# Kernel tuning notes

Measured on AMD Instinct MI355X. Metric: run time of the kernel, lower is better.

The kernel has to match this reference:

```python
import jax, jax.numpy as jnp
import numpy as np


def setup_inputs() -> dict:
    key = jax.random.key(0)
    kx, kq, kk, kv = jax.random.split(key, 4)
    B, S, F, D = 4, 4096, 512, 64
    x = jax.random.normal(kx, (B, S, F), dtype=jnp.float32)
    Wq = jax.random.normal(kq, (F, D), dtype=jnp.float32) * 0.05
    Wk = jax.random.normal(kk, (F, D), dtype=jnp.float32) * 0.05
    Wv = jax.random.normal(kv, (F, D), dtype=jnp.float32) * 0.05
    return {"x": x, "Wq": Wq, "Wk": Wk, "Wv": Wv}


def reference(x, Wq, Wk, Wv):
    # x: [B,S,F]; Wq/Wk/Wv: [F,D]
    q = jnp.einsum('bsf,fd->bsd', x, Wq)
    k = jnp.einsum('bsf,fd->bsd', x, Wk)
    v = jnp.einsum('bsf,fd->bsd', x, Wv)
    scale = 1.0 / jnp.sqrt(jnp.asarray(Wq.shape[-1], dtype=x.dtype))
    scores = jnp.einsum('bqd,bkd->bqk', q, k) * scale  # [B,S,S]
    weights = jax.nn.softmax(scores, axis=-1)
    return jnp.einsum('bqk,bkd->bqd', weights, v)
```

## Files before the change

### kernel.cpp

```cpp
#include <hip/hip_runtime.h>

constexpr int Bc = 4, Sc = 4096, Fc = 512, Dc = 64;
constexpr int SPLIT = 8;
constexpr int KT = 64;
constexpr int TILES = (Sc / SPLIT) / KT;

typedef __attribute__((ext_vector_type(8)))  short  short8;
typedef __attribute__((ext_vector_type(4)))  float  float4v;
typedef __attribute__((ext_vector_type(16))) float  float16v;
typedef __attribute__((ext_vector_type(2)))  unsigned int uint2v;

__device__ inline unsigned short f2bf(float f) {
    union { float f; unsigned u; } v; v.f = f;
    unsigned r = v.u + 0x7FFF + ((v.u >> 16) & 1);
    return (unsigned short)(r >> 16);
}
__device__ inline unsigned pk2(float a, float b) {
    union { float f; unsigned u; } x, y; x.f = a; y.f = b;
    unsigned ra = x.u + 0x7FFF + ((x.u >> 16) & 1);
    unsigned rb = y.u + 0x7FFF + ((y.u >> 16) & 1);
    return (ra >> 16) | (rb & 0xFFFF0000u);
}
__device__ inline unsigned cvtpk2(float lo, float hi) {
    unsigned r;
    asm("v_cvt_pk_bf16_f32 %0, %1, %2" : "=v"(r) : "v"(lo), "v"(hi));
    return r;
}
__device__ inline float exp2fast(float x) {
#if defined(__has_builtin) && __has_builtin(__builtin_amdgcn_exp2f)
    return __builtin_amdgcn_exp2f(x);
#else
    return __expf(x * 0.69314718055994531f);
#endif
}

__device__ inline void swap32(unsigned& a, unsigned& b) {
#if defined(__has_builtin) && __has_builtin(__builtin_amdgcn_permlane32_swap)
    uint2v r = __builtin_amdgcn_permlane32_swap(a, b, false, false);
    a = r[0]; b = r[1];
#else
    unsigned ax = (unsigned)__shfl_xor((int)a, 32);
    unsigned bx = (unsigned)__shfl_xor((int)b, 32);
    int upper = (threadIdx.x & 32) != 0;
    unsigned na = upper ? bx : a;
    unsigned nb = upper ? b  : ax;
    a = na; b = nb;
#endif
}

__global__ __launch_bounds__(256) void prep_kernel(
    const float* __restrict__ Wq, const float* __restrict__ Wk,
    const float* __restrict__ Wv, unsigned short* __restrict__ Wf)
{
    int wi = blockIdx.x * 256 + threadIdx.x;
    int lane = wi & 63;
    int kc = (wi >> 6) & 15;
    int nt = wi >> 10;
    int lm = lane & 15, quad = lane >> 4;
    int n = nt * 16 + lm;
    const float* W = (n < 64) ? Wq : (n < 128) ? Wk : Wv;
    int nc = n & 63;
    float scale = (n < 64) ? 0.18033688011112042f : 1.0f;
    int kbase = kc * 32 + quad * 8;
    union { uint4 v; unsigned short s[8]; } tmp;
    #pragma unroll
    for (int j = 0; j < 8; ++j)
        tmp.s[j] = f2bf(W[(size_t)(kbase + j) * Dc + nc] * scale);
    *(uint4*)&Wf[(size_t)wi * 8] = tmp.v;
}

__global__ __launch_bounds__(256) void qkv_kernel(
    const float* __restrict__ x, const unsigned short* __restrict__ Wf,
    unsigned short* __restrict__ Qb, unsigned short* __restrict__ Kb,
    unsigned short* __restrict__ Vtb)
{
    __shared__ __align__(16) unsigned short Xs[2][16][72];
    __shared__ __align__(16) unsigned short Ot[16][200];
    const int t = threadIdx.x;
    const int lane = t & 63, w = t >> 6;
    const int lm = lane & 15, quad = lane >> 4;
    const int row0 = blockIdx.x * 16;
    const int sr = t >> 4, sc4 = (t & 15) * 4;

    float4 xv;
    auto load_x = [&](int k0) {
        xv = *(const float4*)&x[(size_t)(row0 + sr) * Fc + k0 + sc4];
    };
    load_x(0);

    float4v acc[3];
    #pragma unroll
    for (int n = 0; n < 3; ++n) acc[n] = float4v{0.f, 0.f, 0.f, 0.f};

    int buf = 0;
    #pragma unroll
    for (int k0 = 0; k0 < Fc; k0 += 64, buf ^= 1) {
        uint2 pk;
        pk.x = pk2(xv.x, xv.y); pk.y = pk2(xv.z, xv.w);
        *(uint2*)&Xs[buf][sr][sc4] = pk;
        __syncthreads();
        if (k0 + 64 < Fc) load_x(k0 + 64);

        short8 af[2];
        #pragma unroll
        for (int h = 0; h < 2; ++h)
            af[h] = *(const short8*)&Xs[buf][lm][h * 32 + quad * 8];

        #pragma unroll
        for (int n = 0; n < 3; ++n) {
            const int nt = 3 * w + n;
            #pragma unroll
            for (int h = 0; h < 2; ++h) {
                const int kchunk = (k0 >> 5) + h;
                short8 bf_ = *(const short8*)&Wf[(size_t)((nt * 16 + kchunk) * 64 + lane) * 8];
                acc[n] = __builtin_amdgcn_mfma_f32_16x16x32_bf16(af[h], bf_, acc[n], 0, 0, 0);
            }
        }
    }

    __syncthreads();
    #pragma unroll
    for (int n = 0; n < 3; ++n)
        #pragma unroll
        for (int r = 0; r < 4; ++r)
            Ot[quad * 4 + r][(3 * w + n) * 16 + lm] = f2bf(acc[n][r]);
    __syncthreads();

    {
        const int r2 = t >> 4, c2 = (t & 15) * 4;
        *(uint2*)&Qb[(size_t)(row0 + r2) * Dc + c2] = *(const uint2*)&Ot[r2][c2];
        *(uint2*)&Kb[(size_t)(row0 + r2) * Dc + c2] = *(const uint2*)&Ot[r2][64 + c2];
    }
    {
        const int d = t >> 2, s4 = (t & 3) * 4;
        union { uint2 v; unsigned short s[4]; } tmp;
        #pragma unroll
        for (int j = 0; j < 4; ++j) tmp.s[j] = Ot[s4 + j][128 + d];
        const int bb = row0 >> 12, s0r = row0 & (Sc - 1);
        *(uint2*)&Vtb[((size_t)bb * Dc + d) * Sc + s0r + s4] = tmp.v;
    }
}

__global__ __launch_bounds__(256) void attn_kernel(
    const unsigned short* __restrict__ Qb, const unsigned short* __restrict__ Kb,
    const unsigned short* __restrict__ Vtb,
    float* __restrict__ Op, float* __restrict__ lp)
{
    __shared__ __align__(16) char smem[34816];

    const int t = threadIdx.x;
    const int lane = t & 63, w = t >> 6;
    const int l31 = lane & 31, lh = lane >> 5;
    const int b = blockIdx.y, z = blockIdx.z;
    const int q0 = blockIdx.x * 128 + w * 32;
    const size_t qkbase = (size_t)b * Sc * Dc;
    const size_t vbase  = (size_t)b * Dc * Sc;
    const int k0base = z * (Sc / SPLIT);

    short8 qf[4];
    #pragma unroll
    for (int c = 0; c < 4; ++c)
        qf[c] = *(const short8*)&Qb[qkbase + (size_t)(q0 + l31) * Dc + c * 16 + lh * 8];

    float16v O0, O1;
    #pragma unroll
    for (int r = 0; r < 16; ++r) { O0[r] = 0.f; O1[r] = 0.f; }
    float lA = 0.f, lB = 0.f;

    const int rowInW = lane >> 3;
    const int srcChunk = (lane & 7) ^ rowInW;
    auto stage = [&](int p, int k0) {
        char* base = smem + p * 16384;
        #pragma unroll
        for (int j = 0; j < 2; ++j) {
            const int row = w * 16 + j * 8 + rowInW;
            const unsigned short* gk = Kb + qkbase + (size_t)(k0 + row) * Dc + srcChunk * 8;
            const unsigned short* gv = Vtb + vbase + (size_t)row * Sc + k0 + srcChunk * 8;
            __builtin_amdgcn_global_load_lds(
                (const __attribute__((address_space(1))) void*)gk,
                (__attribute__((address_space(3))) void*)(base + (w * 16 + j * 8) * 128),
                16, 0, 0);
            __builtin_amdgcn_global_load_lds(
                (const __attribute__((address_space(1))) void*)gv,
                (__attribute__((address_space(3))) void*)(base + 8192 + (w * 16 + j * 8) * 128),
                16, 0, 0);
        }
    };

    const int rx = l31 & 7;
    auto rd = [&](const char* buf, int row, int cc) -> short8 {
        return *(const short8*)(buf + row * 128 + (cc ^ rx) * 16);
    };

    auto mk_pb = [&](const float16v& s, int g) -> short8 {
        unsigned X0 = cvtpk2(s[8 * g + 0], s[8 * g + 1]);
        unsigned X1 = cvtpk2(s[8 * g + 2], s[8 * g + 3]);
        unsigned Y0 = cvtpk2(s[8 * g + 4], s[8 * g + 5]);
        unsigned Y1 = cvtpk2(s[8 * g + 6], s[8 * g + 7]);
        swap32(X0, Y0);
        swap32(X1, Y1);
        union { unsigned u[4]; short8 s8; } r;
        r.u[0] = X0; r.u[1] = X1; r.u[2] = Y0; r.u[3] = Y1;
        return r.s8;
    };

    stage(0, k0base);
    __syncthreads();

    int p = 0;
    for (int kt = 0; kt < TILES; ++kt, p ^= 1) {
        if (kt + 1 < TILES) stage(p ^ 1, k0base + (kt + 1) * KT);
        const char* kb = smem + p * 16384;
        const char* vb = kb + 8192;

        float16v s0, s1;
        #pragma unroll
        for (int r = 0; r < 16; ++r) { s0[r] = 0.f; s1[r] = 0.f; }
        __builtin_amdgcn_s_setprio(1);
        #pragma unroll
        for (int c = 0; c < 4; ++c) {
            short8 a0 = rd(kb, l31,      2 * c + lh);
            short8 a1 = rd(kb, 32 + l31, 2 * c + lh);
            s0 = __builtin_amdgcn_mfma_f32_32x32x16_bf16(a0, qf[c], s0, 0, 0, 0);
            s1 = __builtin_amdgcn_mfma_f32_32x32x16_bf16(a1, qf[c], s1, 0, 0, 0);
        }
        __builtin_amdgcn_s_setprio(0);

        #pragma unroll
        for (int r = 0; r < 16; ++r) {
            float p0 = exp2fast(s0[r]); s0[r] = p0; lA += p0;
            float p1 = exp2fast(s1[r]); s1[r] = p1; lB += p1;
        }

        short8 pb0 = mk_pb(s0, 0);
        short8 pb1 = mk_pb(s0, 1);
        short8 pb2 = mk_pb(s1, 0);
        short8 pb3 = mk_pb(s1, 1);

        __builtin_amdgcn_s_setprio(1);
        #pragma unroll
        for (int c = 0; c < 4; ++c) {
            short8 pb  = (c == 0) ? pb0 : (c == 1) ? pb1 : (c == 2) ? pb2 : pb3;
            short8 va0 = rd(vb, l31,      2 * c + lh);
            short8 va1 = rd(vb, 32 + l31, 2 * c + lh);
            O0 = __builtin_amdgcn_mfma_f32_32x32x16_bf16(va0, pb, O0, 0, 0, 0);
            O1 = __builtin_amdgcn_mfma_f32_32x32x16_bf16(va1, pb, O1, 0, 0, 0);
        }
        __builtin_amdgcn_s_setprio(0);

        __syncthreads();
    }

    float l_i = lA + lB;
    l_i += __shfl_xor(l_i, 32);

    float* Of = (float*)(smem + w * 8704);
    #pragma unroll
    for (int r = 0; r < 16; ++r) {
        int d0 = (r & 3) + 8 * (r >> 2) + 4 * lh;
        Of[l31 * 68 + d0]      = O0[r];
        Of[l31 * 68 + 32 + d0] = O1[r];
    }
    const size_t obase = ((size_t)(z * Bc + b) * Sc + q0) * Dc;
    const int qr = lane >> 4, c4 = (lane & 15) * 4;
    #pragma unroll
    for (int i = 0; i < 8; ++i) {
        int q = i * 4 + qr;
        *(float4*)&Op[obase + (size_t)q * Dc + c4] = *(const float4*)&Of[q * 68 + c4];
    }
    if (lane < 32)
        lp[(z * Bc + b) * Sc + q0 + l31] = l_i;
}

__global__ __launch_bounds__(256) void combine_kernel(
    const float* __restrict__ Op, const float* __restrict__ lp,
    float* __restrict__ out)
{
    const int BS = Bc * Sc;
    int tid = blockIdx.x * 256 + threadIdx.x;
    int bq = tid >> 4, dc = (tid & 15) * 4;
    float L = 0.f;
    #pragma unroll
    for (int zz = 0; zz < SPLIT; ++zz) L += lp[zz * BS + bq];
    float inv = 1.f / L;
    size_t o = (size_t)bq * Dc + dc;
    size_t stride = (size_t)BS * Dc;
    float4 r = {0.f, 0.f, 0.f, 0.f};
    #pragma unroll
    for (int zz = 0; zz < SPLIT; ++zz) {
        float4 pz = *(const float4*)&Op[o + zz * stride];
        r.x += pz.x; r.y += pz.y; r.z += pz.z; r.w += pz.w;
    }
    r.x *= inv; r.y *= inv; r.z *= inv; r.w *= inv;
    *(float4*)&out[o] = r;
}

extern "C" void kernel_launch(void* const* d_in, const int* in_sizes, int n_in,
                              void* d_out, int out_size, void* d_ws, size_t ws_size,
                              hipStream_t stream) {
    const float* x  = (const float*)d_in[0];
    const float* Wq = (const float*)d_in[1];
    const float* Wk = (const float*)d_in[2];
    const float* Wv = (const float*)d_in[3];
    float* out = (float*)d_out;

    char* p = (char*)d_ws;
    unsigned short* Wf  = (unsigned short*)p;  p += (size_t)192 * Fc * 2;
    unsigned short* Qb  = (unsigned short*)p;  p += (size_t)Bc * Sc * Dc * 2;
    unsigned short* Kb  = (unsigned short*)p;  p += (size_t)Bc * Sc * Dc * 2;
    unsigned short* Vtb = (unsigned short*)p;  p += (size_t)Bc * Sc * Dc * 2;
    float* lp = (float*)p;                     p += (size_t)SPLIT * Bc * Sc * 4;
    float* Op = (float*)p;

    prep_kernel<<<48, 256, 0, stream>>>(Wq, Wk, Wv, Wf);
    qkv_kernel<<<Bc * Sc / 16, 256, 0, stream>>>(x, Wf, Qb, Kb, Vtb);
    attn_kernel<<<dim3(Sc / 128, Bc, SPLIT), 256, 0, stream>>>(Qb, Kb, Vtb, Op, lp);
    combine_kernel<<<(Bc * Sc * 16) / 256, 256, 0, stream>>>(Op, lp, out);
}
```

Baseline: 120.2 us.

## Split keys across waves within a block and reduce partials in LDS

Each block now handles 32 queries, and its four waves each process a quarter of the key range. Each wave has its own double-buffered LDS slice and waits with vmcnt instead of block barriers. The partial outputs and row sums are combined in shared memory at the end, which removes the separate combine kernel and the global partial-output round trip. A block-index swizzle is added for locality. The cost is a smaller KT tile, so fewer MFMAs per load, plus more LDS per block, which may reduce occupancy.

```diff
diff --git a/kernel.cpp b/kernel.cpp
--- a/kernel.cpp
+++ b/kernel.cpp
@@ -1,9 +1,8 @@
 #include <hip/hip_runtime.h>
 
 constexpr int Bc = 4, Sc = 4096, Fc = 512, Dc = 64;
-constexpr int SPLIT = 8;
-constexpr int KT = 64;
-constexpr int TILES = (Sc / SPLIT) / KT;
+constexpr int KT = 32;
+constexpr int NT = (Sc / 4) / KT;
 
 typedef __attribute__((ext_vector_type(8)))  short  short8;
 typedef __attribute__((ext_vector_type(4)))  float  float4v;
@@ -144,18 +143,21 @@
 __global__ __launch_bounds__(256) void attn_kernel(
     const unsigned short* __restrict__ Qb, const unsigned short* __restrict__ Kb,
     const unsigned short* __restrict__ Vtb,
-    float* __restrict__ Op, float* __restrict__ lp)
+    float* __restrict__ out)
 {
-    __shared__ __align__(16) char smem[34816];
+    __shared__ __align__(16) char smem[65536];
 
     const int t = threadIdx.x;
     const int lane = t & 63, w = t >> 6;
     const int l31 = lane & 31, lh = lane >> 5;
-    const int b = blockIdx.y, z = blockIdx.z;
-    const int q0 = blockIdx.x * 128 + w * 32;
+
+    const int orig = blockIdx.x;
+    const int swz = (orig & 7) * 64 + (orig >> 3);
+    const int b = swz >> 7;
+    const int q0 = (swz & 127) * 32;
     const size_t qkbase = (size_t)b * Sc * Dc;
     const size_t vbase  = (size_t)b * Dc * Sc;
-    const int k0base = z * (Sc / SPLIT);
+    const int kw0 = w * (Sc / 4);
 
     short8 qf[4];
     #pragma unroll
@@ -167,29 +169,33 @@
     for (int r = 0; r < 16; ++r) { O0[r] = 0.f; O1[r] = 0.f; }
     float lA = 0.f, lB = 0.f;
 
-    const int rowInW = lane >> 3;
-    const int srcChunk = (lane & 7) ^ rowInW;
+    char* const slice = smem + w * 16384;
+    const int sk8 = (lane & 7) ^ ((lane >> 3) & 7);
+    const int sv4 = (lane & 3) ^ ((lane >> 3) & 3);
+
     auto stage = [&](int p, int k0) {
-        char* base = smem + p * 16384;
-        #pragma unroll
-        for (int j = 0; j < 2; ++j) {
-            const int row = w * 16 + j * 8 + rowInW;
-            const unsigned short* gk = Kb + qkbase + (size_t)(k0 + row) * Dc + srcChunk * 8;
-            const unsigned short* gv = Vtb + vbase + (size_t)row * Sc + k0 + srcChunk * 8;
+        char* kb = slice + p * 8192;
+        char* vb = kb + 4096;
+        #pragma unroll
+        for (int j = 0; j < 4; ++j) {
+            const int krow = j * 8 + (lane >> 3);
+            const unsigned short* gk = Kb + qkbase + (size_t)(k0 + krow) * Dc + sk8 * 8;
             __builtin_amdgcn_global_load_lds(
                 (const __attribute__((address_space(1))) void*)gk,
-                (__attribute__((address_space(3))) void*)(base + (w * 16 + j * 8) * 128),
-                16, 0, 0);
+                (__attribute__((address_space(3))) void*)(kb + j * 1024), 16, 0, 0);
+            const int vrow = j * 16 + (lane >> 2);
+            const unsigned short* gv = Vtb + vbase + (size_t)vrow * Sc + k0 + sv4 * 8;
             __builtin_amdgcn_global_load_lds(
                 (const __attribute__((address_space(1))) void*)gv,
-                (__attribute__((address_space(3))) void*)(base + 8192 + (w * 16 + j * 8) * 128),
-                16, 0, 0);
-        }
-    };
-
-    const int rx = l31 & 7;
-    auto rd = [&](const char* buf, int row, int cc) -> short8 {
-        return *(const short8*)(buf + row * 128 + (cc ^ rx) * 16);
+                (__attribute__((address_space(3))) void*)(vb + j * 1024), 16, 0, 0);
+        }
+    };
+
+    auto rdK = [&](const char* kb, int row, int cc) -> short8 {
+        return *(const short8*)(kb + row * 128 + ((cc ^ (row & 7)) * 16));
+    };
+    auto rdV = [&](const char* vb, int row, int cc) -> short8 {
+        return *(const short8*)(vb + row * 64 + ((cc ^ ((row >> 1) & 3)) * 16));
     };
 
     auto mk_pb = [&](const float16v& s, int g) -> short8 {
@@ -204,95 +210,89 @@
         return r.s8;
     };
 
-    stage(0, k0base);
-    __syncthreads();
+    stage(0, kw0);
 
     int p = 0;
-    for (int kt = 0; kt < TILES; ++kt, p ^= 1) {
-        if (kt + 1 < TILES) stage(p ^ 1, k0base + (kt + 1) * KT);
-        const char* kb = smem + p * 16384;
-        const char* vb = kb + 8192;
-
-        float16v s0, s1;
-        #pragma unroll
-        for (int r = 0; r < 16; ++r) { s0[r] = 0.f; s1[r] = 0.f; }
+    for (int kt = 0; kt < NT; ++kt, p ^= 1) {
+        if (kt + 1 < NT) {
+            stage(p ^ 1, kw0 + (kt + 1) * KT);
+            asm volatile("s_waitcnt vmcnt(8)" ::: "memory");
+        } else {
+            asm volatile("s_waitcnt vmcnt(0)" ::: "memory");
+        }
+        __builtin_amdgcn_sched_barrier(0);
+        const char* kb = slice + p * 8192;
+        const char* vb = kb + 4096;
+
+        float16v s;
+        #pragma unroll
+        for (int r = 0; r < 16; ++r) s[r] = 0.f;
         __builtin_amdgcn_s_setprio(1);
         #pragma unroll
         for (int c = 0; c < 4; ++c) {
-            short8 a0 = rd(kb, l31,      2 * c + lh);
-            short8 a1 = rd(kb, 32 + l31, 2 * c + lh);
-            s0 = __builtin_amdgcn_mfma_f32_32x32x16_bf16(a0, qf[c], s0, 0, 0, 0);
-            s1 = __builtin_amdgcn_mfma_f32_32x32x16_bf16(a1, qf[c], s1, 0, 0, 0);
+            short8 a = rdK(kb, l31, 2 * c + lh);
+            s = __builtin_amdgcn_mfma_f32_32x32x16_bf16(a, qf[c], s, 0, 0, 0);
         }
         __builtin_amdgcn_s_setprio(0);
 
         #pragma unroll
         for (int r = 0; r < 16; ++r) {
-            float p0 = exp2fast(s0[r]); s0[r] = p0; lA += p0;
-            float p1 = exp2fast(s1[r]); s1[r] = p1; lB += p1;
-        }
-
-        short8 pb0 = mk_pb(s0, 0);
-        short8 pb1 = mk_pb(s0, 1);
-        short8 pb2 = mk_pb(s1, 0);
-        short8 pb3 = mk_pb(s1, 1);
+            float pe = exp2fast(s[r]); s[r] = pe;
+            if (r < 8) lA += pe; else lB += pe;
+        }
+
+        short8 pb0 = mk_pb(s, 0);
+        short8 pb1 = mk_pb(s, 1);
 
         __builtin_amdgcn_s_setprio(1);
         #pragma unroll
-        for (int c = 0; c < 4; ++c) {
-            short8 pb  = (c == 0) ? pb0 : (c == 1) ? pb1 : (c == 2) ? pb2 : pb3;
-            short8 va0 = rd(vb, l31,      2 * c + lh);
-            short8 va1 = rd(vb, 32 + l31, 2 * c + lh);
+        for (int c = 0; c < 2; ++c) {
+            short8 pb  = c ? pb1 : pb0;
+            short8 va0 = rdV(vb, l31,      2 * c + lh);
+            short8 va1 = rdV(vb, 32 + l31, 2 * c + lh);
             O0 = __builtin_amdgcn_mfma_f32_32x32x16_bf16(va0, pb, O0, 0, 0, 0);
             O1 = __builtin_amdgcn_mfma_f32_32x32x16_bf16(va1, pb, O1, 0, 0, 0);
         }
         __builtin_amdgcn_s_setprio(0);
-
-        __syncthreads();
     }
 
     float l_i = lA + lB;
     l_i += __shfl_xor(l_i, 32);
 
-    float* Of = (float*)(smem + w * 8704);
+    float* Of = (float*)slice;
     #pragma unroll
     for (int r = 0; r < 16; ++r) {
         int d0 = (r & 3) + 8 * (r >> 2) + 4 * lh;
         Of[l31 * 68 + d0]      = O0[r];
         Of[l31 * 68 + 32 + d0] = O1[r];
     }
-    const size_t obase = ((size_t)(z * Bc + b) * Sc + q0) * Dc;
-    const int qr = lane >> 4, c4 = (lane & 15) * 4;
-    #pragma unroll
-    for (int i = 0; i < 8; ++i) {
-        int q = i * 4 + qr;
-        *(float4*)&Op[obase + (size_t)q * Dc + c4] = *(const float4*)&Of[q * 68 + c4];
-    }
-    if (lane < 32)
-        lp[(z * Bc + b) * Sc + q0 + l31] = l_i;
-}
-
-__global__ __launch_bounds__(256) void combine_kernel(
-    const float* __restrict__ Op, const float* __restrict__ lp,
-    float* __restrict__ out)
-{
-    const int BS = Bc * Sc;
-    int tid = blockIdx.x * 256 + threadIdx.x;
-    int bq = tid >> 4, dc = (tid & 15) * 4;
-    float L = 0.f;
-    #pragma unroll
-    for (int zz = 0; zz < SPLIT; ++zz) L += lp[zz * BS + bq];
-    float inv = 1.f / L;
-    size_t o = (size_t)bq * Dc + dc;
-    size_t stride = (size_t)BS * Dc;
-    float4 r = {0.f, 0.f, 0.f, 0.f};
-    #pragma unroll
-    for (int zz = 0; zz < SPLIT; ++zz) {
-        float4 pz = *(const float4*)&Op[o + zz * stride];
-        r.x += pz.x; r.y += pz.y; r.z += pz.z; r.w += pz.w;
-    }
-    r.x *= inv; r.y *= inv; r.z *= inv; r.w *= inv;
-    *(float4*)&out[o] = r;
+    float* lw = (float*)(slice + 8704);
+    if (lane < 32) lw[l31] = l_i;
+
+    __syncthreads();
+
+    {
+        const int q = t >> 3, d8 = (t & 7) * 8;
+        float acc8[8];
+        #pragma unroll
+        for (int j = 0; j < 8; ++j) acc8[j] = 0.f;
+        float L = 0.f;
+        #pragma unroll
+        for (int w2 = 0; w2 < 4; ++w2) {
+            const float* OfW = (const float*)(smem + w2 * 16384);
+            const float* lwW = (const float*)(smem + w2 * 16384 + 8704);
+            L += lwW[q];
+            #pragma unroll
+            for (int j = 0; j < 8; ++j) acc8[j] += OfW[q * 68 + d8 + j];
+        }
+        float inv = 1.f / L;
+        float4 o0, o1;
+        o0.x = acc8[0] * inv; o0.y = acc8[1] * inv; o0.z = acc8[2] * inv; o0.w = acc8[3] * inv;
+        o1.x = acc8[4] * inv; o1.y = acc8[5] * inv; o1.z = acc8[6] * inv; o1.w = acc8[7] * inv;
+        float* op = out + ((size_t)b * Sc + q0 + q) * Dc + d8;
+        *(float4*)op = o0;
+        *(float4*)(op + 4) = o1;
+    }
 }
 
 extern "C" void kernel_launch(void* const* d_in, const int* in_sizes, int n_in,
@@ -308,12 +308,9 @@
     unsigned short* Wf  = (unsigned short*)p;  p += (size_t)192 * Fc * 2;
     unsigned short* Qb  = (unsigned short*)p;  p += (size_t)Bc * Sc * Dc * 2;
     unsigned short* Kb  = (unsigned short*)p;  p += (size_t)Bc * Sc * Dc * 2;
-    unsigned short* Vtb = (unsigned short*)p;  p += (size_t)Bc * Sc * Dc * 2;
-    float* lp = (float*)p;                     p += (size_t)SPLIT * Bc * Sc * 4;
-    float* Op = (float*)p;
+    unsigned short* Vtb = (unsigned short*)p;
 
     prep_kernel<<<48, 256, 0, stream>>>(Wq, Wk, Wv, Wf);
     qkv_kernel<<<Bc * Sc / 16, 256, 0, stream>>>(x, Wf, Qb, Kb, Vtb);
-    attn_kernel<<<dim3(Sc / 128, Bc, SPLIT), 256, 0, stream>>>(Qb, Kb, Vtb, Op, lp);
-    combine_kernel<<<(Bc * Sc * 16) / 256, 256, 0, stream>>>(Op, lp, out);
-}
+    attn_kernel<<<dim3(Sc / 32 * Bc), 256, 0, stream>>>(Qb, Kb, Vtb, out);
+}
```

Result: no change. 118.5 us, median of 2 (-1.5%).
